# Performance work log

Measured on AMD Instinct MI355X. Metric: run time of the kernel, lower is better.

The kernel has to match this reference:

```python
import jax, jax.numpy as jnp
import numpy as np

K = 16  # num neighbors


def setup_inputs() -> dict:
    key = jax.random.key(0)
    ks = jax.random.split(key, 10)
    B, N, d_in, d_out = 4, 8192, 64, 128
    h = d_out // 2
    return {
        "xyz": jax.random.normal(ks[0], (B, 3, N), jnp.float32),
        "feature": jax.random.normal(ks[1], (B, d_in, N), jnp.float32),
        "w1": jax.random.normal(ks[2], (h, 10), jnp.float32) * 0.1,
        "b1": jax.random.normal(ks[3], (h,), jnp.float32) * 0.1,
        "w2": jax.random.normal(ks[4], (h, h), jnp.float32) * 0.1,
        "b2": jax.random.normal(ks[5], (h,), jnp.float32) * 0.1,
        "w3": jax.random.normal(ks[6], (h, h), jnp.float32) * 0.1,
        "b3": jax.random.normal(ks[7], (h,), jnp.float32) * 0.1,
        "ws": jax.random.normal(ks[8], (d_out, d_in), jnp.float32) * 0.1,
        "bs": jax.random.normal(ks[9], (d_out,), jnp.float32) * 0.1,
    }


def reference(xyz, feature, w1, b1, w2, b2, w3, b3, ws, bs):
    # xyz: [B,3,N], feature: [B,d_in,N]
    xyz_t = jnp.transpose(xyz, (0, 2, 1))  # [B,N,3]
    sq = jnp.sum(xyz_t * xyz_t, axis=-1)  # [B,N]
    # squared pairwise distance [B,N,N]
    dist = sq[:, :, None] + sq[:, None, :] - 2.0 * jnp.einsum("bnc,bmc->bnm", xyz_t, xyz_t)
    _, idx = jax.lax.top_k(-dist, K)  # smallest-k -> [B,N,K]
    # gather neighbor coords: [B,N,K,3]
    knn_xyz = jax.vmap(lambda pts, ind: pts[ind])(xyz_t, idx)
    center = jnp.broadcast_to(xyz_t[:, :, None, :], knn_xyz.shape)  # [B,N,K,3]
    diff = knn_xyz - center
    dsq = jnp.sum(diff * diff, axis=-1, keepdims=True)  # [B,N,K,1]
    pos = jnp.concatenate([center, knn_xyz, diff, dsq], axis=-1)  # [B,N,K,10]
    # three 1x1 convs over channel dim (no activations, faithful to source)
    h = jnp.einsum("bnkc,oc->bnko", pos, w1) + b1
    h = jnp.einsum("bnkc,oc->bnko", h, w2) + b2
    h = jnp.einsum("bnkc,oc->bnko", h, w3) + b3
    fe = jnp.max(h, axis=2)  # max-pool over neighbors -> [B,N,d_out//2]
    fe = jnp.transpose(fe, (0, 2, 1))  # [B,d_out//2,N]
    shortcut = jnp.einsum("bcn,oc->bon", feature, ws) + bs[None, :, None]
    return jnp.concatenate([fe, fe], axis=1) + shortcut  # [B,d_out,N]
```

## Files before the change

### kernel.cpp

```cpp
#include <hip/hip_runtime.h>

#define B_ 4
#define N_ 8192
#define DIN 64
#define HDIM 64
#define DOUT 128
#define KNN 16
#define QPB 16
#define QPW 4
#define NTHR 256
#define BUFS 64
#define BLOCKS_PER_B (N_ / QPB)

__device__ __forceinline__ int mbcnt64(unsigned long long m) {
  return __builtin_amdgcn_mbcnt_hi((unsigned)(m >> 32),
         __builtin_amdgcn_mbcnt_lo((unsigned)m, 0));
}
__device__ __forceinline__ unsigned mapkey(float d) {
  unsigned u = __float_as_uint(d);
  return (d < 0.0f) ? ~u : (u | 0x80000000u);
}
__device__ __forceinline__ float rf(float x) {
  return __int_as_float(__builtin_amdgcn_readfirstlane(__float_as_int(x)));
}

__device__ __forceinline__
float select16(unsigned* skQ, unsigned short* siQ, int cnt, unsigned short* fout) {
  const int l = threadIdx.x & 63;
  unsigned k = 0xFFFFFFFFu;
  unsigned mi = 0xFFFFu;
  if (l < cnt) { k = skQ[l]; mi = siQ[l]; }
  unsigned p = 0; int r = KNN;
  for (int bit = 31; bit >= 0; bit--) {
    unsigned long long ml = __ballot((int)(((k ^ p) >> bit) == 0u));
    int c0 = __popcll(ml);
    if (r > c0) { p |= (1u << bit); r -= c0; }
  }
  bool isLT = (k < p), isTie = (k == p);
  int tieC = __popcll(__ballot((int)isTie));
  bool keepT = isTie;
  if (tieC != r) {
    unsigned mk = isTie ? mi : 0xFFFFFFFFu;
    unsigned p2 = 0; int r2 = r;
    for (int bit = 15; bit >= 0; bit--) {
      unsigned long long ml = __ballot((int)(((mk ^ p2) >> bit) == 0u));
      int c0 = __popcll(ml);
      if (r2 > c0) { p2 |= (1u << bit); r2 -= c0; }
    }
    keepT = isTie && (mi <= p2);
  }
  bool keep = isLT || keepT;
  unsigned long long km = __ballot((int)keep);
  int rank = mbcnt64(km);
  if (fout) {
    if (keep) fout[rank * QPB] = (unsigned short)mi;
  } else {
    if (keep) { skQ[rank] = k; siQ[rank] = (unsigned short)mi; }
  }
  unsigned fb = (p & 0x80000000u) ? (p & 0x7FFFFFFFu) : ~p;
  return __uint_as_float(fb);
}

__global__ __launch_bounds__(NTHR, 8) void k_lfa(
    const float* __restrict__ xyz, const float* __restrict__ feature,
    const float* __restrict__ w1, const float* __restrict__ b1,
    const float* __restrict__ w2, const float* __restrict__ b2,
    const float* __restrict__ w3, const float* __restrict__ b3,
    const float* __restrict__ wsM, const float* __restrict__ bs,
    float* __restrict__ out) {
  const int blk = blockIdx.x;
  const int b  = blk >> 9;
  const int n0 = (blk & 511) << 4;
  const int t = threadIdx.x;
  const int lane = t & 63;
  const int j = __builtin_amdgcn_readfirstlane(t >> 6);
  const float* xb = xyz + (size_t)b * 3 * N_;
  const float INF = __uint_as_float(0x7f800000u);

  __shared__ alignas(16) unsigned char poolRaw[12800];
  unsigned* skey = (unsigned*)poolRaw;
  unsigned short* sidx = (unsigned short*)(poolRaw + 4096);
  unsigned short* fidx = (unsigned short*)(poolRaw + 6144);
  float4* prmL = (float4*)(poolRaw + 6656);

  {
    float* M2 = (float*)poolRaw;
    float* bbv = (float*)(poolRaw + 2560);
    if (t < HDIM) {
      float r[10];
#pragma unroll
      for (int c = 0; c < 10; c++) r[c] = 0.f;
      float s = b2[t];
      for (int ll = 0; ll < HDIM; ll++) {
        float w = w2[t * HDIM + ll];
#pragma unroll
        for (int c = 0; c < 10; c++) r[c] = fmaf(w, w1[ll * 10 + c], r[c]);
        s = fmaf(w, b1[ll], s);
      }
#pragma unroll
      for (int c = 0; c < 10; c++) M2[t * 10 + c] = r[c];
      bbv[t] = s;
    }
    __syncthreads();
    float4 pv0, pv1;
    if (t < HDIM) {
      float r3[10];
#pragma unroll
      for (int c = 0; c < 10; c++) r3[c] = 0.f;
      float bc = b3[t];
      for (int ll = 0; ll < HDIM; ll++) {
        float w = w3[t * HDIM + ll];
#pragma unroll
        for (int c = 0; c < 10; c++) r3[c] = fmaf(w, M2[ll * 10 + c], r3[c]);
        bc = fmaf(w, bbv[ll], bc);
      }
      pv0 = make_float4(r3[0] - r3[6], r3[1] - r3[7], r3[2] - r3[8], bc);
      pv1 = make_float4(r3[3] + r3[6], r3[4] + r3[7], r3[5] + r3[8], r3[9]);
    }
    __syncthreads();
    if (t < HDIM) { prmL[t] = pv0; prmL[64 + t] = pv1; }
  }

  float qX[QPW], qY[QPW], qZ[QPW], qS[QPW];
#pragma unroll
  for (int i = 0; i < QPW; i++) {
    int mq = n0 + j * QPW + i;
    float x = xb[mq], y = xb[N_ + mq], z = xb[2 * N_ + mq];
    float sq = __fadd_rn(__fadd_rn(__fmul_rn(x, x), __fmul_rn(y, y)), __fmul_rn(z, z));
    qX[i] = rf(x); qY[i] = rf(y); qZ[i] = rf(z); qS[i] = rf(sq);
  }
  float tauF[QPW]; int cntA[QPW];
#pragma unroll
  for (int i = 0; i < QPW; i++) { tauF[i] = INF; cntA[i] = 0; }
  __syncthreads();

  auto process = [&](float cx, float cy, float cz, int base) {
    float cw = __fadd_rn(__fadd_rn(__fmul_rn(cx, cx), __fmul_rn(cy, cy)),
                         __fmul_rn(cz, cz));
    float dd[QPW];
#pragma unroll
    for (int i = 0; i < QPW; i++) {
      float dot = fmaf(cz, qZ[i], fmaf(cy, qY[i], __fmul_rn(cx, qX[i])));
      dd[i] = fmaf(-2.0f, dot, __fadd_rn(qS[i], cw));
    }
#pragma unroll
    for (int i = 0; i < QPW; i++) {
      bool mine = dd[i] < tauF[i];
      unsigned long long hit = __ballot((int)mine);
      if (hit) {
        unsigned* skQ = skey + (j * QPW + i) * BUFS;
        unsigned short* siQ = sidx + (j * QPW + i) * BUFS;
        int h = __popcll(hit);
        int rk = mbcnt64(hit);
        unsigned key = mapkey(dd[i]);
        unsigned short mm = (unsigned short)(base + lane);
        if (cntA[i] + h <= BUFS) {
          if (mine) { skQ[cntA[i] + rk] = key; siQ[cntA[i] + rk] = mm; }
          cntA[i] += h;
          if (cntA[i] == BUFS) {
            tauF[i] = rf(select16(skQ, siQ, BUFS, nullptr));
            cntA[i] = KNN;
          }
        } else {
          unsigned long long rem = hit; bool mrem = mine;
          while (rem) {
            int freeS = BUFS - cntA[i];
            int hh = __popcll(rem);
            int rr = mbcnt64(rem);
            bool wn = mrem && (rr < freeS);
            if (wn) { skQ[cntA[i] + rr] = key; siQ[cntA[i] + rr] = mm; }
            cntA[i] += (hh < freeS) ? hh : freeS;
            if (cntA[i] == BUFS) {
              tauF[i] = rf(select16(skQ, siQ, BUFS, nullptr));
              cntA[i] = KNN;
            }
            mrem = mrem && !wn && (dd[i] < tauF[i]);
            rem = __ballot((int)mrem);
          }
        }
      }
    }
  };

  float x0 = xb[lane],      y0 = xb[N_ + lane],      z0 = xb[2 * N_ + lane];
  float x1 = xb[64 + lane], y1 = xb[N_ + 64 + lane], z1 = xb[2 * N_ + 64 + lane];
  for (int m0 = 0; m0 < N_; m0 += 64) {
    const int mn = (m0 + 128) & (N_ - 1);
    float x2 = xb[mn + lane], y2 = xb[N_ + mn + lane], z2 = xb[2 * N_ + mn + lane];
    process(x0, y0, z0, m0);
    x0 = x1; y0 = y1; z0 = z1;
    x1 = x2; y1 = y2; z1 = z2;
  }
#pragma unroll
  for (int i = 0; i < QPW; i++) {
    select16(skey + (j * QPW + i) * BUFS, sidx + (j * QPW + i) * BUFS,
             cntA[i], fidx + (j * QPW + i));
  }
  __syncthreads();

  const int q = t & 15;
  const int g = t >> 4;
  const float qx = xb[n0 + q], qy = xb[N_ + n0 + q], qz = xb[2 * N_ + n0 + q];
  float* nb = (float*)poolRaw;
  float* feFe = (float*)(poolRaw + 8704);
  {
    int m = fidx[g * QPB + q];
    float x = xb[m], y = xb[N_ + m], z = xb[2 * N_ + m];
    float dx = __fsub_rn(x, qx), dy = __fsub_rn(y, qy), dz = __fsub_rn(z, qz);
    float dsq = __fadd_rn(__fadd_rn(__fmul_rn(dx, dx), __fmul_rn(dy, dy)),
                          __fmul_rn(dz, dz));
    nb[g * QPB + q] = x;
    nb[(16 + g) * QPB + q] = y;
    nb[(32 + g) * QPB + q] = z;
    nb[(48 + g) * QPB + q] = dsq;
  }
  __syncthreads();

  {
    float mx0 = -INF, mx1 = -INF, mx2 = -INF, mx3 = -INF;
    const int c0 = g * 4;
    float4 pB0 = prmL[64 + c0], pB1 = prmL[64 + c0 + 1];
    float4 pB2 = prmL[64 + c0 + 2], pB3 = prmL[64 + c0 + 3];
#pragma unroll
    for (int k = 0; k < KNN; k++) {
      float nx = nb[k * QPB + q], ny = nb[(16 + k) * QPB + q];
      float nz = nb[(32 + k) * QPB + q], nd = nb[(48 + k) * QPB + q];
      mx0 = fmaxf(mx0, fmaf(nz, pB0.z, fmaf(ny, pB0.y, fmaf(nx, pB0.x, __fmul_rn(nd, pB0.w)))));
      mx1 = fmaxf(mx1, fmaf(nz, pB1.z, fmaf(ny, pB1.y, fmaf(nx, pB1.x, __fmul_rn(nd, pB1.w)))));
      mx2 = fmaxf(mx2, fmaf(nz, pB2.z, fmaf(ny, pB2.y, fmaf(nx, pB2.x, __fmul_rn(nd, pB2.w)))));
      mx3 = fmaxf(mx3, fmaf(nz, pB3.z, fmaf(ny, pB3.y, fmaf(nx, pB3.x, __fmul_rn(nd, pB3.w)))));
    }
    float4 pA0 = prmL[c0], pA1 = prmL[c0 + 1], pA2 = prmL[c0 + 2], pA3 = prmL[c0 + 3];
    feFe[(c0 + 0) * QPB + q] = fmaf(qz, pA0.z, fmaf(qy, pA0.y, fmaf(qx, pA0.x, pA0.w))) + mx0;
    feFe[(c0 + 1) * QPB + q] = fmaf(qz, pA1.z, fmaf(qy, pA1.y, fmaf(qx, pA1.x, pA1.w))) + mx1;
    feFe[(c0 + 2) * QPB + q] = fmaf(qz, pA2.z, fmaf(qy, pA2.y, fmaf(qx, pA2.x, pA2.w))) + mx2;
    feFe[(c0 + 3) * QPB + q] = fmaf(qz, pA3.z, fmaf(qy, pA3.y, fmaf(qx, pA3.x, pA3.w))) + mx3;
  }
  __syncthreads();

  float* feL = (float*)poolRaw;
#pragma unroll
  for (int ci = 0; ci < 4; ci++) {
    int c = g * 4 + ci;
    feL[c * QPB + q] = feature[(size_t)(b * DIN + c) * N_ + n0 + q];
  }
  __syncthreads();

  float acc[8];
#pragma unroll
  for (int oi = 0; oi < 8; oi++) acc[oi] = 0.f;
  const float4* wsRow = (const float4*)(wsM + (size_t)g * 8 * DIN);
  for (int c4 = 0; c4 < DIN / 4; c4++) {
    float f0 = feL[(4 * c4 + 0) * QPB + q];
    float f1 = feL[(4 * c4 + 1) * QPB + q];
    float f2 = feL[(4 * c4 + 2) * QPB + q];
    float f3 = feL[(4 * c4 + 3) * QPB + q];
#pragma unroll
    for (int oi = 0; oi < 8; oi++) {
      float4 w = wsRow[oi * (DIN / 4) + c4];
      acc[oi] = fmaf(w.x, f0, acc[oi]);
      acc[oi] = fmaf(w.y, f1, acc[oi]);
      acc[oi] = fmaf(w.z, f2, acc[oi]);
      acc[oi] = fmaf(w.w, f3, acc[oi]);
    }
  }
  float* ob = out + (size_t)b * DOUT * N_ + n0 + q;
#pragma unroll
  for (int oi = 0; oi < 8; oi++) {
    int o = g * 8 + oi;
    ob[(size_t)o * N_] = acc[oi] + bs[o] + feFe[(o & 63) * QPB + q];
  }
}

extern "C" void kernel_launch(void* const* d_in, const int* in_sizes, int n_in,
                              void* d_out, int out_size, void* d_ws, size_t ws_size,
                              hipStream_t stream) {
  const float* xyz     = (const float*)d_in[0];
  const float* feature = (const float*)d_in[1];
  const float* w1 = (const float*)d_in[2];
  const float* b1 = (const float*)d_in[3];
  const float* w2 = (const float*)d_in[4];
  const float* b2 = (const float*)d_in[5];
  const float* w3 = (const float*)d_in[6];
  const float* b3 = (const float*)d_in[7];
  const float* wsM = (const float*)d_in[8];
  const float* bs  = (const float*)d_in[9];
  float* out = (float*)d_out;

  hipLaunchKernelGGL(k_lfa, dim3(B_ * BLOCKS_PER_B), dim3(NTHR), 0, stream,
                     xyz, feature, w1, b1, w2, b2, w3, b3, wsM, bs, out);
}
```

Measured before the change: 292.4 us.

## Sort points by x and prune KNN search with slab-distance bounds

Adds a pre-pass kernel that bucket-sorts each batch's points by x coordinate and packs them as float4 (x,y,z,|p|^2) with original indices. The KNN kernel then processes queries in sorted order, seeds its candidate buffer from the query's own batch, and expands left and right over 64-point batches. It stops once the x-gap squared exceeds the current 16th-nearest threshold, replacing the brute-force scan over all N points. The epilogue is split into a third kernel that reads neighbor indices from workspace, at the cost of two extra launches, global round-trips, and a sort with a single block per batch. Ties now use <=, and the 1.0001 slack on the pruning threshold guards against rounding.

Result: slower. 330.1 us (+12.9%).

```diff
diff --git a/kernel.cpp b/kernel.cpp
--- a/kernel.cpp
+++ b/kernel.cpp
@@ -6,11 +6,12 @@
 #define HDIM 64
 #define DOUT 128
 #define KNN 16
+#define NBUCK 2048
 #define QPB 16
 #define QPW 4
 #define NTHR 256
 #define BUFS 64
-#define BLOCKS_PER_B (N_ / QPB)
+#define NBATCH (N_ / 64)
 
 __device__ __forceinline__ int mbcnt64(unsigned long long m) {
   return __builtin_amdgcn_mbcnt_hi((unsigned)(m >> 32),
@@ -25,7 +26,7 @@
 }
 
 __device__ __forceinline__
-float select16(unsigned* skQ, unsigned short* siQ, int cnt, unsigned short* fout) {
+float select16(unsigned* skQ, unsigned short* siQ, int cnt, unsigned short* gout) {
   const int l = threadIdx.x & 63;
   unsigned k = 0xFFFFFFFFu;
   unsigned mi = 0xFFFFu;
@@ -52,110 +53,207 @@
   bool keep = isLT || keepT;
   unsigned long long km = __ballot((int)keep);
   int rank = mbcnt64(km);
-  if (fout) {
-    if (keep) fout[rank * QPB] = (unsigned short)mi;
+  if (gout) {
+    if (keep) gout[rank] = mi;
   } else {
-    if (keep) { skQ[rank] = k; siQ[rank] = (unsigned short)mi; }
+    if (keep) { skQ[rank] = k; siQ[rank] = mi; }
   }
   unsigned fb = (p & 0x80000000u) ? (p & 0x7FFFFFFFu) : ~p;
   return __uint_as_float(fb);
 }
 
-__global__ __launch_bounds__(NTHR, 8) void k_lfa(
-    const float* __restrict__ xyz, const float* __restrict__ feature,
+__global__ __launch_bounds__(1024) void k_sort(
+    const float* __restrict__ xyz,
     const float* __restrict__ w1, const float* __restrict__ b1,
     const float* __restrict__ w2, const float* __restrict__ b2,
     const float* __restrict__ w3, const float* __restrict__ b3,
-    const float* __restrict__ wsM, const float* __restrict__ bs,
-    float* __restrict__ out) {
+    float4* __restrict__ pk4, unsigned short* __restrict__ sid,
+    float4* __restrict__ prm) {
+  const int t = threadIdx.x;
+  __shared__ unsigned histA[NBUCK];
+  __shared__ unsigned histB[NBUCK];
+  __shared__ float rmm[32];
+
+  if (blockIdx.x == 4) {
+    float* M2 = (float*)histA;
+    float* bbv = (float*)histB;
+    if (t < HDIM) {
+      float r[10];
+#pragma unroll
+      for (int c = 0; c < 10; c++) r[c] = 0.f;
+      float s = b2[t];
+      for (int l = 0; l < HDIM; l++) {
+        float w = w2[t * HDIM + l];
+#pragma unroll
+        for (int c = 0; c < 10; c++) r[c] = fmaf(w, w1[l * 10 + c], r[c]);
+        s = fmaf(w, b1[l], s);
+      }
+#pragma unroll
+      for (int c = 0; c < 10; c++) M2[t * 10 + c] = r[c];
+      bbv[t] = s;
+    }
+    __syncthreads();
+    if (t < HDIM) {
+      float r3[10];
+#pragma unroll
+      for (int c = 0; c < 10; c++) r3[c] = 0.f;
+      float bc = b3[t];
+      for (int l = 0; l < HDIM; l++) {
+        float w = w3[t * HDIM + l];
+#pragma unroll
+        for (int c = 0; c < 10; c++) r3[c] = fmaf(w, M2[l * 10 + c], r3[c]);
+        bc = fmaf(w, bbv[l], bc);
+      }
+      prm[t]      = make_float4(r3[0] - r3[6], r3[1] - r3[7], r3[2] - r3[8], bc);
+      prm[64 + t] = make_float4(r3[3] + r3[6], r3[4] + r3[7], r3[5] + r3[8], r3[9]);
+    }
+    return;
+  }
+
+  const int b = blockIdx.x;
+  const float* xb = xyz + (size_t)b * 3 * N_;
+  float xs[8];
+  float lmin = 1e30f, lmax = -1e30f;
+#pragma unroll
+  for (int r = 0; r < 8; r++) {
+    xs[r] = xb[r * 1024 + t];
+    lmin = fminf(lmin, xs[r]); lmax = fmaxf(lmax, xs[r]);
+  }
+  for (int off = 32; off; off >>= 1) {
+    lmin = fminf(lmin, __shfl_xor(lmin, off));
+    lmax = fmaxf(lmax, __shfl_xor(lmax, off));
+  }
+  const int wid = t >> 6;
+  if ((t & 63) == 0) { rmm[wid] = lmin; rmm[16 + wid] = lmax; }
+  histA[t] = 0; histA[t + 1024] = 0;
+  __syncthreads();
+  if (t == 0) {
+    float mn = rmm[0], mx = rmm[16];
+    for (int w = 1; w < 16; w++) { mn = fminf(mn, rmm[w]); mx = fmaxf(mx, rmm[16 + w]); }
+    rmm[0] = mn; rmm[16] = mx;
+  }
+  __syncthreads();
+  const float mn = rmm[0];
+  const float range = rmm[16] - mn;
+  const float scale = (range > 0.f) ? ((float)NBUCK / range) : 0.f;
+  int bk[8];
+#pragma unroll
+  for (int r = 0; r < 8; r++) {
+    int v = (int)((xs[r] - mn) * scale);
+    bk[r] = v > (NBUCK - 1) ? (NBUCK - 1) : (v < 0 ? 0 : v);
+    atomicAdd(&histA[bk[r]], 1u);
+  }
+  __syncthreads();
+  unsigned* src = histA; unsigned* dst = histB;
+  for (int off = 1; off < NBUCK; off <<= 1) {
+    for (int i = t; i < NBUCK; i += 1024) {
+      unsigned v = src[i];
+      if (i >= off) v += src[i - off];
+      dst[i] = v;
+    }
+    __syncthreads();
+    unsigned* tmp = src; src = dst; dst = tmp;
+  }
+  for (int i = t; i < NBUCK; i += 1024) dst[i] = i ? src[i - 1] : 0u;
+  __syncthreads();
+#pragma unroll
+  for (int r = 0; r < 8; r++) {
+    int m = r * 1024 + t;
+    float x = xs[r], y = xb[N_ + m], z = xb[2 * N_ + m];
+    float sq = __fadd_rn(__fadd_rn(__fmul_rn(x, x), __fmul_rn(y, y)), __fmul_rn(z, z));
+    unsigned pos = atomicAdd(&dst[bk[r]], 1u);
+    pk4[((size_t)b << 13) + pos] = make_float4(x, y, z, sq);
+    sid[((size_t)b << 13) + pos] = (unsigned short)m;
+  }
+}
+
+__global__ __launch_bounds__(NTHR, 6) void k_knn(
+    const float4* __restrict__ pk4, const unsigned short* __restrict__ sid,
+    unsigned short* __restrict__ fidxG) {
   const int blk = blockIdx.x;
   const int b  = blk >> 9;
-  const int n0 = (blk & 511) << 4;
+  const int s0 = (blk & 511) << 4;
   const int t = threadIdx.x;
   const int lane = t & 63;
   const int j = __builtin_amdgcn_readfirstlane(t >> 6);
-  const float* xb = xyz + (size_t)b * 3 * N_;
+  const float4* pkb = pk4 + ((size_t)b << 13);
+  const unsigned short* sdb = sid + ((size_t)b << 13);
   const float INF = __uint_as_float(0x7f800000u);
 
-  __shared__ alignas(16) unsigned char poolRaw[12800];
-  unsigned* skey = (unsigned*)poolRaw;
-  unsigned short* sidx = (unsigned short*)(poolRaw + 4096);
-  unsigned short* fidx = (unsigned short*)(poolRaw + 6144);
-  float4* prmL = (float4*)(poolRaw + 6656);
-
+  __shared__ unsigned skey[QPB * BUFS];
+  __shared__ unsigned short sidxS[QPB * BUFS];
+
+  float qX[QPW], qY[QPW], qZ[QPW], qS[QPW]; int qN[QPW];
+#pragma unroll
+  for (int i = 0; i < QPW; i++) {
+    int p = s0 + j * QPW + i;
+    float4 qv = pkb[p];
+    qX[i] = rf(qv.x); qY[i] = rf(qv.y); qZ[i] = rf(qv.z); qS[i] = rf(qv.w);
+    qN[i] = __builtin_amdgcn_readfirstlane((int)sdb[p]);
+  }
+  const float qxmin = fminf(fminf(qX[0], qX[1]), fminf(qX[2], qX[3]));
+  const float qxmax = fmaxf(fmaxf(qX[0], qX[1]), fmaxf(qX[2], qX[3]));
+  float tauF[QPW]; int cntA[QPW];
+
+  const int start = (s0 + j * QPW) >> 6;
   {
-    float* M2 = (float*)poolRaw;
-    float* bbv = (float*)(poolRaw + 2560);
-    if (t < HDIM) {
-      float r[10];
-#pragma unroll
-      for (int c = 0; c < 10; c++) r[c] = 0.f;
-      float s = b2[t];
-      for (int ll = 0; ll < HDIM; ll++) {
-        float w = w2[t * HDIM + ll];
-#pragma unroll
-        for (int c = 0; c < 10; c++) r[c] = fmaf(w, w1[ll * 10 + c], r[c]);
-        s = fmaf(w, b1[ll], s);
-      }
-#pragma unroll
-      for (int c = 0; c < 10; c++) M2[t * 10 + c] = r[c];
-      bbv[t] = s;
-    }
-    __syncthreads();
-    float4 pv0, pv1;
-    if (t < HDIM) {
-      float r3[10];
-#pragma unroll
-      for (int c = 0; c < 10; c++) r3[c] = 0.f;
-      float bc = b3[t];
-      for (int ll = 0; ll < HDIM; ll++) {
-        float w = w3[t * HDIM + ll];
-#pragma unroll
-        for (int c = 0; c < 10; c++) r3[c] = fmaf(w, M2[ll * 10 + c], r3[c]);
-        bc = fmaf(w, bbv[ll], bc);
-      }
-      pv0 = make_float4(r3[0] - r3[6], r3[1] - r3[7], r3[2] - r3[8], bc);
-      pv1 = make_float4(r3[3] + r3[6], r3[4] + r3[7], r3[5] + r3[8], r3[9]);
-    }
-    __syncthreads();
-    if (t < HDIM) { prmL[t] = pv0; prmL[64 + t] = pv1; }
-  }
-
-  float qX[QPW], qY[QPW], qZ[QPW], qS[QPW];
-#pragma unroll
-  for (int i = 0; i < QPW; i++) {
-    int mq = n0 + j * QPW + i;
-    float x = xb[mq], y = xb[N_ + mq], z = xb[2 * N_ + mq];
-    float sq = __fadd_rn(__fadd_rn(__fmul_rn(x, x), __fmul_rn(y, y)), __fmul_rn(z, z));
-    qX[i] = rf(x); qY[i] = rf(y); qZ[i] = rf(z); qS[i] = rf(sq);
-  }
-  float tauF[QPW]; int cntA[QPW];
-#pragma unroll
-  for (int i = 0; i < QPW; i++) { tauF[i] = INF; cntA[i] = 0; }
-  __syncthreads();
-
-  auto process = [&](float cx, float cy, float cz, int base) {
-    float cw = __fadd_rn(__fadd_rn(__fmul_rn(cx, cx), __fmul_rn(cy, cy)),
-                         __fmul_rn(cz, cz));
+    float4 c = pkb[start * 64 + lane];
+    unsigned short mid = sdb[start * 64 + lane];
+#pragma unroll
+    for (int i = 0; i < QPW; i++) {
+      float dot = fmaf(c.z, qZ[i], fmaf(c.y, qY[i], __fmul_rn(c.x, qX[i])));
+      float d = fmaf(-2.0f, dot, __fadd_rn(qS[i], c.w));
+      skey[(j * QPW + i) * BUFS + lane] = mapkey(d);
+      sidxS[(j * QPW + i) * BUFS + lane] = mid;
+    }
+#pragma unroll
+    for (int i = 0; i < QPW; i++) {
+      tauF[i] = rf(select16(skey + (j * QPW + i) * BUFS,
+                            sidxS + (j * QPW + i) * BUFS, BUFS, nullptr));
+      cntA[i] = KNN;
+    }
+  }
+
+  int bl = start - 1, br = start + 1;
+  for (;;) {
+    bool lo = (bl >= 0), ro = (br < NBATCH);
+    if (!(lo | ro)) break;
+    float tmax = fmaxf(fmaxf(tauF[0], tauF[1]), fmaxf(tauF[2], tauF[3])) * 1.0001f;
+    float dl = INF, dr = INF;
+    if (lo) {
+      float e = pkb[bl * 64 + 63].x;
+      dl = __fsub_rn(qxmin, e);
+      if (dl > 0.f && __fmul_rn(dl, dl) > tmax) { lo = false; bl = -1; }
+    }
+    if (ro) {
+      float e = pkb[br * 64].x;
+      dr = __fsub_rn(e, qxmax);
+      if (dr > 0.f && __fmul_rn(dr, dr) > tmax) { ro = false; br = NBATCH; }
+    }
+    if (!(lo | ro)) break;
+    int pb;
+    if (lo && (!ro || dl <= dr)) { pb = bl; bl--; } else { pb = br; br++; }
+
+    float4 c = pkb[pb * 64 + lane];
+    unsigned short mid = sdb[pb * 64 + lane];
     float dd[QPW];
 #pragma unroll
     for (int i = 0; i < QPW; i++) {
-      float dot = fmaf(cz, qZ[i], fmaf(cy, qY[i], __fmul_rn(cx, qX[i])));
-      dd[i] = fmaf(-2.0f, dot, __fadd_rn(qS[i], cw));
+      float dot = fmaf(c.z, qZ[i], fmaf(c.y, qY[i], __fmul_rn(c.x, qX[i])));
+      dd[i] = fmaf(-2.0f, dot, __fadd_rn(qS[i], c.w));
     }
 #pragma unroll
     for (int i = 0; i < QPW; i++) {
-      bool mine = dd[i] < tauF[i];
+      bool mine = dd[i] <= tauF[i];
       unsigned long long hit = __ballot((int)mine);
       if (hit) {
         unsigned* skQ = skey + (j * QPW + i) * BUFS;
-        unsigned short* siQ = sidx + (j * QPW + i) * BUFS;
+        unsigned short* siQ = sidxS + (j * QPW + i) * BUFS;
         int h = __popcll(hit);
         int rk = mbcnt64(hit);
         unsigned key = mapkey(dd[i]);
-        unsigned short mm = (unsigned short)(base + lane);
         if (cntA[i] + h <= BUFS) {
-          if (mine) { skQ[cntA[i] + rk] = key; siQ[cntA[i] + rk] = mm; }
+          if (mine) { skQ[cntA[i] + rk] = key; siQ[cntA[i] + rk] = mid; }
           cntA[i] += h;
           if (cntA[i] == BUFS) {
             tauF[i] = rf(select16(skQ, siQ, BUFS, nullptr));
@@ -168,81 +266,82 @@
             int hh = __popcll(rem);
             int rr = mbcnt64(rem);
             bool wn = mrem && (rr < freeS);
-            if (wn) { skQ[cntA[i] + rr] = key; siQ[cntA[i] + rr] = mm; }
+            if (wn) { skQ[cntA[i] + rr] = key; siQ[cntA[i] + rr] = mid; }
             cntA[i] += (hh < freeS) ? hh : freeS;
             if (cntA[i] == BUFS) {
               tauF[i] = rf(select16(skQ, siQ, BUFS, nullptr));
               cntA[i] = KNN;
             }
-            mrem = mrem && !wn && (dd[i] < tauF[i]);
+            mrem = mrem && !wn && (dd[i] <= tauF[i]);
             rem = __ballot((int)mrem);
           }
         }
       }
     }
-  };
-
-  float x0 = xb[lane],      y0 = xb[N_ + lane],      z0 = xb[2 * N_ + lane];
-  float x1 = xb[64 + lane], y1 = xb[N_ + 64 + lane], z1 = xb[2 * N_ + 64 + lane];
-  for (int m0 = 0; m0 < N_; m0 += 64) {
-    const int mn = (m0 + 128) & (N_ - 1);
-    float x2 = xb[mn + lane], y2 = xb[N_ + mn + lane], z2 = xb[2 * N_ + mn + lane];
-    process(x0, y0, z0, m0);
-    x0 = x1; y0 = y1; z0 = z1;
-    x1 = x2; y1 = y2; z1 = z2;
   }
 #pragma unroll
   for (int i = 0; i < QPW; i++) {
-    select16(skey + (j * QPW + i) * BUFS, sidx + (j * QPW + i) * BUFS,
-             cntA[i], fidx + (j * QPW + i));
-  }
-  __syncthreads();
-
+    select16(skey + (j * QPW + i) * BUFS, sidxS + (j * QPW + i) * BUFS,
+             cntA[i], fidxG + ((((size_t)b << 13) + qN[i]) << 4));
+  }
+}
+
+__global__ __launch_bounds__(256, 8) void k_epi(
+    const float* __restrict__ xyz, const float* __restrict__ feature,
+    const float4* __restrict__ prm, const float* __restrict__ wsM,
+    const float* __restrict__ bs, const unsigned short* __restrict__ fidxG,
+    float* __restrict__ out) {
+  const int blk = blockIdx.x;
+  const int b  = blk >> 9;
+  const int n0 = (blk & 511) << 4;
+  const int t = threadIdx.x;
   const int q = t & 15;
   const int g = t >> 4;
+  const float* xb = xyz + (size_t)b * 3 * N_;
+  const float INF = __uint_as_float(0x7f800000u);
+
+  __shared__ float nb[64 * 16];
+  __shared__ float feFe[64 * 16];
+  __shared__ float feL[64 * 16];
+
   const float qx = xb[n0 + q], qy = xb[N_ + n0 + q], qz = xb[2 * N_ + n0 + q];
-  float* nb = (float*)poolRaw;
-  float* feFe = (float*)(poolRaw + 8704);
   {
-    int m = fidx[g * QPB + q];
+    int m = fidxG[((((size_t)b << 13) + n0 + q) << 4) + g];
     float x = xb[m], y = xb[N_ + m], z = xb[2 * N_ + m];
     float dx = __fsub_rn(x, qx), dy = __fsub_rn(y, qy), dz = __fsub_rn(z, qz);
     float dsq = __fadd_rn(__fadd_rn(__fmul_rn(dx, dx), __fmul_rn(dy, dy)),
                           __fmul_rn(dz, dz));
-    nb[g * QPB + q] = x;
-    nb[(16 + g) * QPB + q] = y;
-    nb[(32 + g) * QPB + q] = z;
-    nb[(48 + g) * QPB + q] = dsq;
+    nb[g * 16 + q] = x;
+    nb[(16 + g) * 16 + q] = y;
+    nb[(32 + g) * 16 + q] = z;
+    nb[(48 + g) * 16 + q] = dsq;
   }
   __syncthreads();
 
   {
     float mx0 = -INF, mx1 = -INF, mx2 = -INF, mx3 = -INF;
     const int c0 = g * 4;
-    float4 pB0 = prmL[64 + c0], pB1 = prmL[64 + c0 + 1];
-    float4 pB2 = prmL[64 + c0 + 2], pB3 = prmL[64 + c0 + 3];
+    float4 pB0 = prm[64 + c0], pB1 = prm[64 + c0 + 1];
+    float4 pB2 = prm[64 + c0 + 2], pB3 = prm[64 + c0 + 3];
 #pragma unroll
     for (int k = 0; k < KNN; k++) {
-      float nx = nb[k * QPB + q], ny = nb[(16 + k) * QPB + q];
-      float nz = nb[(32 + k) * QPB + q], nd = nb[(48 + k) * QPB + q];
+      float nx = nb[k * 16 + q], ny = nb[(16 + k) * 16 + q];
+      float nz = nb[(32 + k) * 16 + q], nd = nb[(48 + k) * 16 + q];
       mx0 = fmaxf(mx0, fmaf(nz, pB0.z, fmaf(ny, pB0.y, fmaf(nx, pB0.x, __fmul_rn(nd, pB0.w)))));
       mx1 = fmaxf(mx1, fmaf(nz, pB1.z, fmaf(ny, pB1.y, fmaf(nx, pB1.x, __fmul_rn(nd, pB1.w)))));
       mx2 = fmaxf(mx2, fmaf(nz, pB2.z, fmaf(ny, pB2.y, fmaf(nx, pB2.x, __fmul_rn(nd, pB2.w)))));
       mx3 = fmaxf(mx3, fmaf(nz, pB3.z, fmaf(ny, pB3.y, fmaf(nx, pB3.x, __fmul_rn(nd, pB3.w)))));
     }
-    float4 pA0 = prmL[c0], pA1 = prmL[c0 + 1], pA2 = prmL[c0 + 2], pA3 = prmL[c0 + 3];
-    feFe[(c0 + 0) * QPB + q] = fmaf(qz, pA0.z, fmaf(qy, pA0.y, fmaf(qx, pA0.x, pA0.w))) + mx0;
-    feFe[(c0 + 1) * QPB + q] = fmaf(qz, pA1.z, fmaf(qy, pA1.y, fmaf(qx, pA1.x, pA1.w))) + mx1;
-    feFe[(c0 + 2) * QPB + q] = fmaf(qz, pA2.z, fmaf(qy, pA2.y, fmaf(qx, pA2.x, pA2.w))) + mx2;
-    feFe[(c0 + 3) * QPB + q] = fmaf(qz, pA3.z, fmaf(qy, pA3.y, fmaf(qx, pA3.x, pA3.w))) + mx3;
-  }
-  __syncthreads();
-
-  float* feL = (float*)poolRaw;
+    float4 pA0 = prm[c0], pA1 = prm[c0 + 1], pA2 = prm[c0 + 2], pA3 = prm[c0 + 3];
+    feFe[(c0 + 0) * 16 + q] = fmaf(qz, pA0.z, fmaf(qy, pA0.y, fmaf(qx, pA0.x, pA0.w))) + mx0;
+    feFe[(c0 + 1) * 16 + q] = fmaf(qz, pA1.z, fmaf(qy, pA1.y, fmaf(qx, pA1.x, pA1.w))) + mx1;
+    feFe[(c0 + 2) * 16 + q] = fmaf(qz, pA2.z, fmaf(qy, pA2.y, fmaf(qx, pA2.x, pA2.w))) + mx2;
+    feFe[(c0 + 3) * 16 + q] = fmaf(qz, pA3.z, fmaf(qy, pA3.y, fmaf(qx, pA3.x, pA3.w))) + mx3;
+  }
 #pragma unroll
   for (int ci = 0; ci < 4; ci++) {
     int c = g * 4 + ci;
-    feL[c * QPB + q] = feature[(size_t)(b * DIN + c) * N_ + n0 + q];
+    feL[c * 16 + q] = feature[(size_t)(b * DIN + c) * N_ + n0 + q];
   }
   __syncthreads();
 
@@ -251,10 +350,10 @@
   for (int oi = 0; oi < 8; oi++) acc[oi] = 0.f;
   const float4* wsRow = (const float4*)(wsM + (size_t)g * 8 * DIN);
   for (int c4 = 0; c4 < DIN / 4; c4++) {
-    float f0 = feL[(4 * c4 + 0) * QPB + q];
-    float f1 = feL[(4 * c4 + 1) * QPB + q];
-    float f2 = feL[(4 * c4 + 2) * QPB + q];
-    float f3 = feL[(4 * c4 + 3) * QPB + q];
+    float f0 = feL[(4 * c4 + 0) * 16 + q];
+    float f1 = feL[(4 * c4 + 1) * 16 + q];
+    float f2 = feL[(4 * c4 + 2) * 16 + q];
+    float f3 = feL[(4 * c4 + 3) * 16 + q];
 #pragma unroll
     for (int oi = 0; oi < 8; oi++) {
       float4 w = wsRow[oi * (DIN / 4) + c4];
@@ -268,7 +367,7 @@
 #pragma unroll
   for (int oi = 0; oi < 8; oi++) {
     int o = g * 8 + oi;
-    ob[(size_t)o * N_] = acc[oi] + bs[o] + feFe[(o & 63) * QPB + q];
+    ob[(size_t)o * N_] = acc[oi] + bs[o] + feFe[(o & 63) * 16 + q];
   }
 }
 
@@ -287,6 +386,15 @@
   const float* bs  = (const float*)d_in[9];
   float* out = (float*)d_out;
 
-  hipLaunchKernelGGL(k_lfa, dim3(B_ * BLOCKS_PER_B), dim3(NTHR), 0, stream,
-                     xyz, feature, w1, b1, w2, b2, w3, b3, wsM, bs, out);
-}
+  float4* prm = (float4*)d_ws;
+  float4* pk4 = (float4*)((char*)d_ws + 4096);
+  unsigned short* sid = (unsigned short*)((char*)d_ws + 528384);
+  unsigned short* fidxG = (unsigned short*)((char*)d_ws + 593920);
+
+  hipLaunchKernelGGL(k_sort, dim3(5), dim3(1024), 0, stream,
+                     xyz, w1, b1, w2, b2, w3, b3, pk4, sid, prm);
+  hipLaunchKernelGGL(k_knn, dim3(B_ * 512), dim3(NTHR), 0, stream,
+                     pk4, sid, fidxG);
+  hipLaunchKernelGGL(k_epi, dim3(B_ * 512), dim3(256), 0, stream,
+                     xyz, feature, prm, wsM, bs, fidxG, out);
+}
```
